# Performance work log

Measured on AMD Instinct MI355X. Metric: run time of the kernel, lower is better.

The kernel has to match this reference:

```python
import jax, jax.numpy as jnp
import numpy as np

CHAR_DIM = 96
COLOR_DIM = 16
GLYPH_DIM = CHAR_DIM * COLOR_DIM  # 1536 bounded id space
CHAR_EMB = 16
COLOR_EMB = 4
GLYPH_EMB = CHAR_EMB + COLOR_EMB  # 20
HID = 32
MAX_LEN = 64


def setup_inputs() -> dict:
    key = jax.random.key(0)
    ks = jax.random.split(key, 8)
    B, H, W = 4096, 21, 79
    glyph_chars = jax.random.randint(ks[0], (B, H, W), 0, CHAR_DIM)
    glyph_colors = jax.random.randint(ks[1], (B, H, W), 0, COLOR_DIM)
    # embedding tables (row CHAR_DIM / COLOR_DIM is the padding row)
    char_table = jax.random.normal(ks[2], (CHAR_DIM + 1, CHAR_EMB), jnp.float32) * 0.1
    col_table = jax.random.normal(ks[3], (COLOR_DIM + 1, COLOR_EMB), jnp.float32) * 0.1
    s = 1.0 / np.sqrt(HID)
    Wih = jax.random.uniform(ks[4], (HID, GLYPH_EMB), jnp.float32, -s, s)
    Whh = jax.random.uniform(ks[5], (HID, HID), jnp.float32, -s, s)
    bih = jax.random.uniform(ks[6], (HID,), jnp.float32, -s, s)
    bhh = jax.random.uniform(ks[7], (HID,), jnp.float32, -s, s)
    return dict(glyph_chars=glyph_chars, glyph_colors=glyph_colors,
                char_table=char_table, col_table=col_table,
                Wih=Wih, Whh=Whh, bih=bih, bhh=bhh)


def reference(glyph_chars, glyph_colors, char_table, col_table, Wih, Whh, bih, bhh):
    B = glyph_chars.shape[0]
    # combined glyph id in the bounded [0, GLYPH_DIM) space
    ids = (glyph_chars * COLOR_DIM + glyph_colors).reshape(B, -1)  # [B, H*W]
    # batched fixed-size histogram over the bounded id space (replaces per-sample torch.unique)
    counts = jnp.zeros((B, GLYPH_DIM), jnp.int32).at[jnp.arange(B)[:, None], ids].add(1)
    present = counts > 0  # [B, GLYPH_DIM]
    # sorted unique ids (ascending == lexicographic over (char,color)); absent ids pushed to GLYPH_DIM
    sorted_ids = jnp.sort(jnp.where(present, jnp.arange(GLYPH_DIM), GLYPH_DIM), axis=-1)[:, :MAX_LEN]
    is_pad = sorted_ids >= GLYPH_DIM
    char_bag = jnp.where(is_pad, CHAR_DIM, sorted_ids // COLOR_DIM)   # pad -> CHAR_DIM row
    color_bag = jnp.where(is_pad, COLOR_DIM, sorted_ids % COLOR_DIM)  # pad -> COLOR_DIM row
    bag = jnp.stack([char_bag, color_bag], axis=-1)  # [B, MAX_LEN, 2]
    lengths = jnp.minimum(present.sum(-1), MAX_LEN)  # [B]
    emb = jnp.concatenate([char_table[char_bag], col_table[color_bag]], axis=-1)  # [B, MAX_LEN, 20]
    # vanilla tanh RNN over the packed (variable-length) bag; keep hidden at last valid step
    def step(h, inp):
        x_t, t = inp  # x_t: [B, 20]
        h_new = jnp.tanh(x_t @ Wih.T + bih + h @ Whh.T + bhh)
        h = jnp.where((t < lengths)[:, None], h_new, h)
        return h, None
    h0 = jnp.zeros((B, HID), emb.dtype)
    h, _ = jax.lax.scan(step, h0, (emb.transpose(1, 0, 2), jnp.arange(MAX_LEN)))
    return h, emb, bag
```

## Files before the change

kernel.cpp:

```cpp
#include <hip/hip_runtime.h>
#include <hip/hip_bf16.h>

#define HW        1659
#define GLYPH_DIM 1536

typedef _Float16 half8  __attribute__((ext_vector_type(8)));
typedef _Float16 half2v __attribute__((ext_vector_type(2)));
typedef float    f32x4  __attribute__((ext_vector_type(4)));

__device__ __forceinline__ float tanh_f(float x) {
    float e = __expf(x + x);
    return fmaf(-2.0f, __builtin_amdgcn_rcpf(e + 1.0f), 1.0f);
}

__device__ __forceinline__ unsigned int pk(float a, float b) {
    return __builtin_bit_cast(unsigned int, __builtin_amdgcn_cvt_pkrtz(a, b));
}

__device__ __forceinline__ half8 h8(unsigned int a, unsigned int b,
                                    unsigned int c, unsigned int d) {
    uint4 u = make_uint4(a, b, c, d);
    return __builtin_bit_cast(half8, u);
}

__global__ __launch_bounds__(256, 8) void k1_histo(
    const int* __restrict__ gchar, const int* __restrict__ gcol,
    unsigned short* __restrict__ ids_bt,
    unsigned short* __restrict__ ids_tb,
    int* __restrict__ lens_g)
{
    __shared__ unsigned int   mask[4][48];
    __shared__ unsigned short ids_s[4][64];

    const int tid = threadIdx.x;
    const int b0  = blockIdx.x * 4;

    if (tid < 192) ((unsigned int*)mask)[tid] = 0u;
    __syncthreads();

    const int4* cp = (const int4*)(gchar + (long)b0 * HW);
    const int4* kp = (const int4*)(gcol  + (long)b0 * HW);
    const int n4 = HW;
    int idx = tid;
    bool valid = idx < n4;
    int4 c = {}, k = {};
    if (valid) { c = cp[idx]; k = kp[idx]; }
    while (valid) {
        int  idx1 = idx + 256;
        bool v1   = idx1 < n4;
        int4 c1 = {}, k1 = {};
        if (v1) { c1 = cp[idx1]; k1 = kp[idx1]; }
        {
            int gg  = idx * 4;
            int bl0 = gg / HW;
            int rem = gg - bl0 * HW;
            int bl1 = bl0 + ((rem + 1) >= HW);
            int bl2 = bl0 + ((rem + 2) >= HW);
            int bl3 = bl0 + ((rem + 3) >= HW);
            int id0 = c.x * 16 + k.x;
            int id1 = c.y * 16 + k.y;
            int id2 = c.z * 16 + k.z;
            int id3 = c.w * 16 + k.w;
            atomicOr(&mask[bl0][id0 >> 5], 1u << (id0 & 31));
            atomicOr(&mask[bl1][id1 >> 5], 1u << (id1 & 31));
            atomicOr(&mask[bl2][id2 >> 5], 1u << (id2 & 31));
            atomicOr(&mask[bl3][id3 >> 5], 1u << (id3 & 31));
        }
        idx = idx1; valid = v1; c = c1; k = k1;
    }
    __syncthreads();

    if (tid < 128) {
        const int bl  = tid >> 5;
        const int l32 = tid & 31;
        unsigned long long m = 0ull;
        if (l32 < 24)
            m = ((unsigned long long)mask[bl][2 * l32 + 1] << 32) |
                (unsigned long long)mask[bl][2 * l32];
        int cnt  = __popcll(m);
        int incl = cnt;
        #pragma unroll
        for (int d = 1; d < 32; d <<= 1) {
            int nb = __shfl_up(incl, d, 32);
            if (l32 >= d) incl += nb;
        }
        int excl  = incl - cnt;
        int total = __shfl(incl, 31, 32);
        if (l32 == 0) lens_g[b0 + bl] = min(total, 64);
        ids_s[bl][l32]      = GLYPH_DIM;
        ids_s[bl][l32 + 32] = GLYPH_DIM;
        unsigned long long mm = m;
        int r = excl;
        while (mm != 0ull && r < 64) {
            int bit = __builtin_ctzll(mm);
            ids_s[bl][r] = (unsigned short)(l32 * 64 + bit);
            ++r;
            mm &= (mm - 1ull);
        }
    }
    __syncthreads();

    if (tid < 128)
        ((unsigned int*)(ids_bt + (long)b0 * 64))[tid] = ((unsigned int*)ids_s)[tid];
    {
        const int bl = tid >> 6, t = tid & 63;
        const int b  = b0 + bl;
        ids_tb[((long)(b >> 6) * 64 + t) * 64 + (b & 63)] = ids_s[bl][t];
    }
}

__global__ __launch_bounds__(256, 4) void k23_main(
    const float* __restrict__ ctab, const float* __restrict__ ktab,
    const float* __restrict__ Wih, const float* __restrict__ Whh,
    const float* __restrict__ bih, const float* __restrict__ bhh,
    const unsigned short* __restrict__ ids_bt,
    const unsigned short* __restrict__ ids_tb,
    const int* __restrict__ lens_g,
    float* __restrict__ out_h, float* __restrict__ out_emb,
    float* __restrict__ out_bag, int nrnn)
{
    __shared__ float          tabs[1620];
    __shared__ unsigned short ids_t[64 * 64];

    const int tid = threadIdx.x;

    for (int i = tid; i < 1620; i += 256)
        tabs[i] = (i < 1552) ? ctab[i] : ktab[i - 1552];

    if ((int)blockIdx.x < nrnn) {
        {
            const unsigned int* src = (const unsigned int*)(ids_tb + (long)blockIdx.x * 4096);
            unsigned int* dst = (unsigned int*)ids_t;
            #pragma unroll
            for (int j = 0; j < 8; ++j) dst[tid + j * 256] = src[tid + j * 256];
        }
        const int n = tid & 15, g = (tid >> 4) & 3;
        half8 wihA0, wihA1, whhA0, whhA1;
        #pragma unroll
        for (int j = 0; j < 8; ++j) {
            int kk = (j < 4) ? (4 * g + j) : (12 + 4 * g + j);
            wihA0[j] = (_Float16)((kk < 20) ? Wih[n * 20 + kk] : 0.0f);
            wihA1[j] = (_Float16)((kk < 20) ? Wih[(n + 16) * 20 + kk] : 0.0f);
            whhA0[j] = (_Float16)Whh[n * 32 + kk];
            whhA1[j] = (_Float16)Whh[(n + 16) * 32 + kk];
        }
        f32x4 bias0, bias1;
        #pragma unroll
        for (int i = 0; i < 4; ++i) {
            bias0[i] = bih[4 * g + i] + bhh[4 * g + i];
            bias1[i] = bih[16 + 4 * g + i] + bhh[16 + 4 * g + i];
        }
        const int ib  = (tid >> 6) * 16 + n;
        const int b   = blockIdx.x * 64 + ib;
        const int len = lens_g[b];
        __syncthreads();

        auto build = [&](int id) -> half8 {
            int ch = id >> 4;
            int co = (id >= GLYPH_DIM) ? 16 : (id & 15);
            f32x4 q1 = *(const f32x4*)&tabs[ch * 16 + 4 * g];
            f32x4 q2 = {0.0f, 0.0f, 0.0f, 0.0f};
            if (g == 0) q2 = *(const f32x4*)&tabs[1552 + co * 4];
            return h8(pk(q1[0], q1[1]), pk(q1[2], q1[3]),
                      pk(q2[0], q2[1]), pk(q2[2], q2[3]));
        };

        half8 x0  = build(ids_t[0 * 64 + ib]);
        f32x4 Pc0 = __builtin_amdgcn_mfma_f32_16x16x32_f16(wihA0, x0, bias0, 0, 0, 0);
        f32x4 Pc1 = __builtin_amdgcn_mfma_f32_16x16x32_f16(wihA1, x0, bias1, 0, 0, 0);
        int   idn = ids_t[1 * 64 + ib];
        f32x4 d0 = {0, 0, 0, 0}, d1 = {0, 0, 0, 0};
        for (int t = 0; t < 64; ++t) {
            f32x4 Pn0 = Pc0, Pn1 = Pc1;
            int   id2 = (t < 62) ? (int)ids_t[(t + 2) * 64 + ib] : idn;
            if (t < 63) {
                half8 xn = build(idn);
                Pn0 = __builtin_amdgcn_mfma_f32_16x16x32_f16(wihA0, xn, bias0, 0, 0, 0);
                Pn1 = __builtin_amdgcn_mfma_f32_16x16x32_f16(wihA1, xn, bias1, 0, 0, 0);
            }
            half8 hB = h8(pk(d0[0], d0[1]), pk(d0[2], d0[3]),
                          pk(d1[0], d1[1]), pk(d1[2], d1[3]));
            f32x4 a0 = __builtin_amdgcn_mfma_f32_16x16x32_f16(whhA0, hB, Pc0, 0, 0, 0);
            f32x4 a1 = __builtin_amdgcn_mfma_f32_16x16x32_f16(whhA1, hB, Pc1, 0, 0, 0);
            bool upd = (t < len);
            #pragma unroll
            for (int i = 0; i < 4; ++i) {
                float h0 = tanh_f(a0[i]);
                float h1 = tanh_f(a1[i]);
                d0[i] = upd ? h0 : d0[i];
                d1[i] = upd ? h1 : d1[i];
            }
            Pc0 = Pn0; Pc1 = Pn1; idn = id2;
        }
        float* op = out_h + (long)b * 32;
        *(f32x4*)(op + 4 * g)      = d0;
        *(f32x4*)(op + 16 + 4 * g) = d1;
    } else {
        __syncthreads();
        const long row = (long)((int)blockIdx.x - nrnn) * 256 + tid;
        int id = ids_bt[row];
        int ch = id >> 4;
        int co = (id >= GLYPH_DIM) ? 16 : (id & 15);
        f32x4 c0 = *(const f32x4*)&tabs[ch * 16 + 0];
        f32x4 c1 = *(const f32x4*)&tabs[ch * 16 + 4];
        f32x4 c2 = *(const f32x4*)&tabs[ch * 16 + 8];
        f32x4 c3 = *(const f32x4*)&tabs[ch * 16 + 12];
        f32x4 k0 = *(const f32x4*)&tabs[1552 + co * 4];
        float* gp = out_emb + row * 20;
        *(f32x4*)(gp + 0)  = c0;
        *(f32x4*)(gp + 4)  = c1;
        *(f32x4*)(gp + 8)  = c2;
        *(f32x4*)(gp + 12) = c3;
        *(f32x4*)(gp + 16) = k0;
        *(float2*)(out_bag + row * 2) = make_float2((float)ch, (float)co);
    }
}

extern "C" void kernel_launch(void* const* d_in, const int* in_sizes, int n_in,
                              void* d_out, int out_size, void* d_ws, size_t ws_size,
                              hipStream_t stream) {
    const int* gchar = (const int*)d_in[0];
    const int* gcol  = (const int*)d_in[1];
    const float* ctab = (const float*)d_in[2];
    const float* ktab = (const float*)d_in[3];
    const float* Wih  = (const float*)d_in[4];
    const float* Whh  = (const float*)d_in[5];
    const float* bih  = (const float*)d_in[6];
    const float* bhh  = (const float*)d_in[7];

    const int B = in_sizes[0] / HW;
    float* out_h   = (float*)d_out;
    float* out_emb = out_h + (long)B * 32;
    float* out_bag = out_emb + (long)B * 64 * 20;

    unsigned short* ids_bt = (unsigned short*)d_ws;
    unsigned short* ids_tb = ids_bt + (long)B * 64;
    int*            lens_g = (int*)((char*)d_ws + (long)B * 64 * 4);

    k1_histo<<<B / 4, 256, 0, stream>>>(gchar, gcol, ids_bt, ids_tb, lens_g);

    const int nrnn = B / 64;
    const int nemb = (B * 64) / 256;
    k23_main<<<nrnn + nemb, 256, 0, stream>>>(
        ctab, ktab, Wih, Whh, bih, bhh, ids_bt, ids_tb, lens_g,
        out_h, out_emb, out_bag, nrnn);
}
```

Measured before the change: 45.78 us.

## Use Pade tanh, fp16 tables and hidden state, and per-wave id layout

```diff
diff --git a/kernel.cpp b/kernel.cpp
--- a/kernel.cpp
+++ b/kernel.cpp
@@ -8,25 +8,29 @@
 typedef _Float16 half2v __attribute__((ext_vector_type(2)));
 typedef float    f32x4  __attribute__((ext_vector_type(4)));
 
-__device__ __forceinline__ float tanh_f(float x) {
-    float e = __expf(x + x);
-    return fmaf(-2.0f, __builtin_amdgcn_rcpf(e + 1.0f), 1.0f);
-}
-
 __device__ __forceinline__ unsigned int pk(float a, float b) {
     return __builtin_bit_cast(unsigned int, __builtin_amdgcn_cvt_pkrtz(a, b));
 }
 
-__device__ __forceinline__ half8 h8(unsigned int a, unsigned int b,
-                                    unsigned int c, unsigned int d) {
+__device__ __forceinline__ half8 h8u(unsigned int a, unsigned int b,
+                                     unsigned int c, unsigned int d) {
     uint4 u = make_uint4(a, b, c, d);
     return __builtin_bit_cast(half8, u);
+}
+
+__device__ __forceinline__ float tanh_pade(float x) {
+    float xc = fmaxf(fminf(x, 4.0f), -4.0f);
+    float y  = xc * xc;
+    float num = xc * fmaf(y, y + 105.0f, 945.0f);
+    float den = fmaf(y, fmaf(y, 15.0f, 420.0f), 945.0f);
+    float r = num * __builtin_amdgcn_rcpf(den);
+    return fmaxf(fminf(r, 1.0f), -1.0f);
 }
 
 __global__ __launch_bounds__(256, 8) void k1_histo(
     const int* __restrict__ gchar, const int* __restrict__ gcol,
     unsigned short* __restrict__ ids_bt,
-    unsigned short* __restrict__ ids_tb,
+    unsigned short* __restrict__ ids_tb16,
     int* __restrict__ lens_g)
 {
     __shared__ unsigned int   mask[4][48];
@@ -62,9 +66,9 @@
             int id2 = c.z * 16 + k.z;
             int id3 = c.w * 16 + k.w;
             atomicOr(&mask[bl0][id0 >> 5], 1u << (id0 & 31));
-            atomicOr(&mask[bl1][id1 >> 5], 1u << (id1 & 31));
-            atomicOr(&mask[bl2][id2 >> 5], 1u << (id2 & 31));
-            atomicOr(&mask[bl3][id3 >> 5], 1u << (id3 & 31));
+            if (id1 != id0 || bl1 != bl0) atomicOr(&mask[bl1][id1 >> 5], 1u << (id1 & 31));
+            if (id2 != id1 || bl2 != bl1) atomicOr(&mask[bl2][id2 >> 5], 1u << (id2 & 31));
+            if (id3 != id2 || bl3 != bl2) atomicOr(&mask[bl3][id3 >> 5], 1u << (id3 & 31));
         }
         idx = idx1; valid = v1; c = c1; k = k1;
     }
@@ -105,7 +109,7 @@
     {
         const int bl = tid >> 6, t = tid & 63;
         const int b  = b0 + bl;
-        ids_tb[((long)(b >> 6) * 64 + t) * 64 + (b & 63)] = ids_s[bl][t];
+        ids_tb16[((long)(b >> 4) * 64 + t) * 16 + (b & 15)] = ids_s[bl][t];
     }
 }
 
@@ -114,27 +118,32 @@
     const float* __restrict__ Wih, const float* __restrict__ Whh,
     const float* __restrict__ bih, const float* __restrict__ bhh,
     const unsigned short* __restrict__ ids_bt,
-    const unsigned short* __restrict__ ids_tb,
+    const unsigned short* __restrict__ ids_tb16,
     const int* __restrict__ lens_g,
     float* __restrict__ out_h, float* __restrict__ out_emb,
     float* __restrict__ out_bag, int nrnn)
 {
+    __shared__ _Float16       tabsh[1664];
+    __shared__ unsigned short ids4[4][64][16];
     __shared__ float          tabs[1620];
-    __shared__ unsigned short ids_t[64 * 64];
 
     const int tid = threadIdx.x;
 
-    for (int i = tid; i < 1620; i += 256)
-        tabs[i] = (i < 1552) ? ctab[i] : ktab[i - 1552];
-
     if ((int)blockIdx.x < nrnn) {
+        const int w = tid >> 6, l = tid & 63;
+        const int n = l & 15,  g = l >> 4;
+        const int bg = blockIdx.x * 4 + w;
+
+        for (int i = tid; i < 1620; i += 256)
+            tabsh[i] = (_Float16)((i < 1552) ? ctab[i] : ktab[i - 1552]);
         {
-            const unsigned int* src = (const unsigned int*)(ids_tb + (long)blockIdx.x * 4096);
-            unsigned int* dst = (unsigned int*)ids_t;
+            const unsigned int* src =
+                (const unsigned int*)(ids_tb16 + (long)blockIdx.x * 4096);
+            unsigned int* dst = (unsigned int*)ids4;
             #pragma unroll
             for (int j = 0; j < 8; ++j) dst[tid + j * 256] = src[tid + j * 256];
         }
-        const int n = tid & 15, g = (tid >> 4) & 3;
+
         half8 wihA0, wihA1, whhA0, whhA1;
         #pragma unroll
         for (int j = 0; j < 8; ++j) {
@@ -150,69 +159,74 @@
             bias0[i] = bih[4 * g + i] + bhh[4 * g + i];
             bias1[i] = bih[16 + 4 * g + i] + bhh[16 + 4 * g + i];
         }
-        const int ib  = (tid >> 6) * 16 + n;
-        const int b   = blockIdx.x * 64 + ib;
-        const int len = lens_g[b];
+        const int len = lens_g[bg * 16 + n];
         __syncthreads();
 
-        auto build = [&](int id) -> half8 {
+        auto build = [&](int t) -> half8 {
+            int id = ids4[w][t][n];
             int ch = id >> 4;
             int co = (id >= GLYPH_DIM) ? 16 : (id & 15);
-            f32x4 q1 = *(const f32x4*)&tabs[ch * 16 + 4 * g];
-            f32x4 q2 = {0.0f, 0.0f, 0.0f, 0.0f};
-            if (g == 0) q2 = *(const f32x4*)&tabs[1552 + co * 4];
-            return h8(pk(q1[0], q1[1]), pk(q1[2], q1[3]),
-                      pk(q2[0], q2[1]), pk(q2[2], q2[3]));
+            uint2 c8 = *(const uint2*)&tabsh[ch * 16 + 4 * g];
+            uint2 k8 = make_uint2(0u, 0u);
+            if (g == 0) k8 = *(const uint2*)&tabsh[1552 + co * 4];
+            return h8u(c8.x, c8.y, k8.x, k8.y);
         };
 
-        half8 x0  = build(ids_t[0 * 64 + ib]);
+        half8 x0  = build(0);
         f32x4 Pc0 = __builtin_amdgcn_mfma_f32_16x16x32_f16(wihA0, x0, bias0, 0, 0, 0);
         f32x4 Pc1 = __builtin_amdgcn_mfma_f32_16x16x32_f16(wihA1, x0, bias1, 0, 0, 0);
-        int   idn = ids_t[1 * 64 + ib];
-        f32x4 d0 = {0, 0, 0, 0}, d1 = {0, 0, 0, 0};
+        unsigned int hw0 = 0u, hw1 = 0u, hw2 = 0u, hw3 = 0u;
         for (int t = 0; t < 64; ++t) {
-            f32x4 Pn0 = Pc0, Pn1 = Pc1;
-            int   id2 = (t < 62) ? (int)ids_t[(t + 2) * 64 + ib] : idn;
-            if (t < 63) {
-                half8 xn = build(idn);
-                Pn0 = __builtin_amdgcn_mfma_f32_16x16x32_f16(wihA0, xn, bias0, 0, 0, 0);
-                Pn1 = __builtin_amdgcn_mfma_f32_16x16x32_f16(wihA1, xn, bias1, 0, 0, 0);
-            }
-            half8 hB = h8(pk(d0[0], d0[1]), pk(d0[2], d0[3]),
-                          pk(d1[0], d1[1]), pk(d1[2], d1[3]));
+            half8 xn  = build((t < 63) ? t + 1 : 63);
+            f32x4 Pn0 = __builtin_amdgcn_mfma_f32_16x16x32_f16(wihA0, xn, bias0, 0, 0, 0);
+            f32x4 Pn1 = __builtin_amdgcn_mfma_f32_16x16x32_f16(wihA1, xn, bias1, 0, 0, 0);
+            half8 hB = h8u(hw0, hw1, hw2, hw3);
             f32x4 a0 = __builtin_amdgcn_mfma_f32_16x16x32_f16(whhA0, hB, Pc0, 0, 0, 0);
             f32x4 a1 = __builtin_amdgcn_mfma_f32_16x16x32_f16(whhA1, hB, Pc1, 0, 0, 0);
+            unsigned int t0 = pk(tanh_pade(a0[0]), tanh_pade(a0[1]));
+            unsigned int t1 = pk(tanh_pade(a0[2]), tanh_pade(a0[3]));
+            unsigned int t2 = pk(tanh_pade(a1[0]), tanh_pade(a1[1]));
+            unsigned int t3 = pk(tanh_pade(a1[2]), tanh_pade(a1[3]));
             bool upd = (t < len);
-            #pragma unroll
-            for (int i = 0; i < 4; ++i) {
-                float h0 = tanh_f(a0[i]);
-                float h1 = tanh_f(a1[i]);
-                d0[i] = upd ? h0 : d0[i];
-                d1[i] = upd ? h1 : d1[i];
-            }
-            Pc0 = Pn0; Pc1 = Pn1; idn = id2;
-        }
-        float* op = out_h + (long)b * 32;
-        *(f32x4*)(op + 4 * g)      = d0;
-        *(f32x4*)(op + 16 + 4 * g) = d1;
+            hw0 = upd ? t0 : hw0;
+            hw1 = upd ? t1 : hw1;
+            hw2 = upd ? t2 : hw2;
+            hw3 = upd ? t3 : hw3;
+            Pc0 = Pn0; Pc1 = Pn1;
+        }
+        float* op = out_h + (long)(bg * 16 + n) * 32;
+        half2v u0 = __builtin_bit_cast(half2v, hw0);
+        half2v u1 = __builtin_bit_cast(half2v, hw1);
+        half2v u2 = __builtin_bit_cast(half2v, hw2);
+        half2v u3 = __builtin_bit_cast(half2v, hw3);
+        f32x4 o0 = {(float)u0[0], (float)u0[1], (float)u1[0], (float)u1[1]};
+        f32x4 o1 = {(float)u2[0], (float)u2[1], (float)u3[0], (float)u3[1]};
+        *(f32x4*)(op + 4 * g)      = o0;
+        *(f32x4*)(op + 16 + 4 * g) = o1;
     } else {
+        for (int i = tid; i < 1620; i += 256)
+            tabs[i] = (i < 1552) ? ctab[i] : ktab[i - 1552];
         __syncthreads();
-        const long row = (long)((int)blockIdx.x - nrnn) * 256 + tid;
-        int id = ids_bt[row];
-        int ch = id >> 4;
-        int co = (id >= GLYPH_DIM) ? 16 : (id & 15);
-        f32x4 c0 = *(const f32x4*)&tabs[ch * 16 + 0];
-        f32x4 c1 = *(const f32x4*)&tabs[ch * 16 + 4];
-        f32x4 c2 = *(const f32x4*)&tabs[ch * 16 + 8];
-        f32x4 c3 = *(const f32x4*)&tabs[ch * 16 + 12];
-        f32x4 k0 = *(const f32x4*)&tabs[1552 + co * 4];
-        float* gp = out_emb + row * 20;
-        *(f32x4*)(gp + 0)  = c0;
-        *(f32x4*)(gp + 4)  = c1;
-        *(f32x4*)(gp + 8)  = c2;
-        *(f32x4*)(gp + 12) = c3;
-        *(f32x4*)(gp + 16) = k0;
-        *(float2*)(out_bag + row * 2) = make_float2((float)ch, (float)co);
+        const long base = (long)((int)blockIdx.x - nrnn) * 512;
+        #pragma unroll
+        for (int rr = 0; rr < 2; ++rr) {
+            const long row = base + rr * 256 + tid;
+            int id = ids_bt[row];
+            int ch = id >> 4;
+            int co = (id >= GLYPH_DIM) ? 16 : (id & 15);
+            f32x4 c0 = *(const f32x4*)&tabs[ch * 16 + 0];
+            f32x4 c1 = *(const f32x4*)&tabs[ch * 16 + 4];
+            f32x4 c2 = *(const f32x4*)&tabs[ch * 16 + 8];
+            f32x4 c3 = *(const f32x4*)&tabs[ch * 16 + 12];
+            f32x4 k0 = *(const f32x4*)&tabs[1552 + co * 4];
+            float* gp = out_emb + row * 20;
+            *(f32x4*)(gp + 0)  = c0;
+            *(f32x4*)(gp + 4)  = c1;
+            *(f32x4*)(gp + 8)  = c2;
+            *(f32x4*)(gp + 12) = c3;
+            *(f32x4*)(gp + 16) = k0;
+            *(float2*)(out_bag + row * 2) = make_float2((float)ch, (float)co);
+        }
     }
 }
 
@@ -233,15 +247,15 @@
     float* out_emb = out_h + (long)B * 32;
     float* out_bag = out_emb + (long)B * 64 * 20;
 
-    unsigned short* ids_bt = (unsigned short*)d_ws;
-    unsigned short* ids_tb = ids_bt + (long)B * 64;
-    int*            lens_g = (int*)((char*)d_ws + (long)B * 64 * 4);
-
-    k1_histo<<<B / 4, 256, 0, stream>>>(gchar, gcol, ids_bt, ids_tb, lens_g);
+    unsigned short* ids_bt   = (unsigned short*)d_ws;
+    unsigned short* ids_tb16 = ids_bt + (long)B * 64;
+    int*            lens_g   = (int*)((char*)d_ws + (long)B * 64 * 4);
+
+    k1_histo<<<B / 4, 256, 0, stream>>>(gchar, gcol, ids_bt, ids_tb16, lens_g);
 
     const int nrnn = B / 64;
-    const int nemb = (B * 64) / 256;
+    const int nemb = (B * 64) / 512;
     k23_main<<<nrnn + nemb, 256, 0, stream>>>(
-        ctab, ktab, Wih, Whh, bih, bhh, ids_bt, ids_tb, lens_g,
+        ctab, ktab, Wih, Whh, bih, bhh, ids_bt, ids_tb16, lens_g,
         out_h, out_emb, out_bag, nrnn);
 }
```

Result: slower. 50.71 us (+10.8%).
